# Kernel optimization log

Hardware: AMD Instinct MI355X
Metric: run time of the kernel (lower is better)

Reference implementation:

```python
import jax, jax.numpy as jnp
import numpy as np

B, C, H, W = 8, 256, 32, 32
N = H * W  # 1024; conv1 maps C -> N channels so all bmms are [B,N,N]


def setup_inputs() -> dict:
    key = jax.random.key(0)
    ks = jax.random.split(key, 11)
    s = 0.02  # weight scale to keep softmax logits in a sane range
    return {
        "x":     jax.random.normal(ks[0], (B, C, H, W), jnp.float32),
        "w1":    jax.random.normal(ks[1], (N, C), jnp.float32) * s,
        "b1":    jax.random.normal(ks[2], (N,), jnp.float32) * s,
        "wq":    jax.random.normal(ks[3], (N, N), jnp.float32) * s,
        "bq":    jax.random.normal(ks[4], (N,), jnp.float32) * s,
        "wv":    jax.random.normal(ks[5], (N, N), jnp.float32) * s,
        "bv":    jax.random.normal(ks[6], (N,), jnp.float32) * s,
        "w2":    jax.random.normal(ks[7], (C, N), jnp.float32) * s,
        "b2":    jax.random.normal(ks[8], (C,), jnp.float32) * s,
        "alpha": jax.random.normal(ks[9], (1,), jnp.float32),
        "beta":  jax.random.normal(ks[10], (1,), jnp.float32),
    }


def reference(x, w1, b1, wq, bq, wv, bv, w2, b2, alpha, beta):
    b, c, h, w = x.shape
    n = h * w
    # 1x1 convs as channel matmuls
    x1 = jnp.einsum('bchw,nc->bnhw', x, w1) + b1[None, :, None, None]  # [B,N,H,W]
    g = (jnp.einsum('bnhw,mn->bmhw', x1, wq) + bq[None, :, None, None]).reshape(b, n, n)
    r = (jnp.einsum('bnhw,mn->bmhw', x1, wv) + bv[None, :, None, None]).reshape(b, n, n)
    xf = x1.reshape(b, n, n)          # m^T in the torch code: [B, N_chan, HW]
    m = xf.transpose(0, 2, 1)         # m: [B, HW, N_chan]
    # spatial attention: z_s = softmax(m^T @ g)
    z_s = jax.nn.softmax(jnp.matmul(xf, g), axis=-1)            # [B,N,N]
    # channel attention: z_c = softmax(g^T @ m)
    z_c = jax.nn.softmax(jnp.matmul(g.transpose(0, 2, 1), m), axis=-1)  # [B,N,N]
    p_s = jnp.matmul(z_s, r)                                    # [B,N,HW]
    p_c = jnp.matmul(z_c, m).transpose(0, 2, 1)                 # [B,N,HW]
    p = (alpha[0] * p_s + beta[0] * p_c).reshape(b, n, h, w)
    out = jnp.einsum('bnhw,cn->bchw', p, w2) + b2[None, :, None, None]
    return out
```

## Files before the change

### kernel.cpp

```cpp
#include <hip/hip_runtime.h>
#include <hip/hip_bf16.h>


typedef __attribute__((ext_vector_type(4))) float f4;
typedef __attribute__((ext_vector_type(8))) short s8;
typedef __attribute__((ext_vector_type(4))) unsigned short us4;
typedef __attribute__((ext_vector_type(8))) unsigned short us8;

__device__ __forceinline__ unsigned short f2bf(float f) {
    __hip_bfloat16 h = __float2bfloat16(f);
    return __builtin_bit_cast(unsigned short, h);
}
__device__ __forceinline__ float bf2f(unsigned short u) {
    unsigned int x = ((unsigned int)u) << 16;
    return __builtin_bit_cast(float, x);
}

#define GAS(p) ((const __attribute__((address_space(1))) unsigned int*)(p))
#define LAS(p) ((__attribute__((address_space(3))) unsigned int*)(p))

__global__ __launch_bounds__(256) void prep(
    const float* __restrict__ w1, const float* __restrict__ wq,
    const float* __restrict__ wv, const float* __restrict__ w2,
    unsigned short* __restrict__ w1b, unsigned short* __restrict__ wqb,
    unsigned short* __restrict__ wvb, unsigned short* __restrict__ w2b,
    const float* __restrict__ bq, const float* __restrict__ bv,
    float* __restrict__ biasqv,
    const float* __restrict__ x, unsigned short* __restrict__ xT)
{
    __shared__ float tl[32][33];
    if (blockIdx.x < 2562) {
        long i = (long)blockIdx.x * 256 + threadIdx.x;
        if (i >= 655360) {
            long j = i - 655360;
            if (j < 512) {
                f4 v = (j < 256) ? ((const f4*)bq)[j] : ((const f4*)bv)[j - 256];
                ((f4*)biasqv)[j] = v;
            }
            return;
        }
        const float* src; unsigned short* dst; long base;
        if (i < 65536)               { src = w1; dst = w1b; base = 0; }
        else if (i < 65536+262144)   { src = wq; dst = wqb; base = 65536; }
        else if (i < 65536+524288)   { src = wv; dst = wvb; base = 65536+262144; }
        else                         { src = w2; dst = w2b; base = 65536+524288; }
        long j = i - base;
        f4 v = ((const f4*)src)[j];
        us4 o;
        #pragma unroll
        for (int k = 0; k < 4; ++k) o[k] = f2bf(v[k]);
        ((us4*)dst)[j] = o;
    } else {
        const int idx = blockIdx.x - 2562;
        const int q0 = (idx & 31) * 32;
        const int c0 = ((idx >> 5) & 7) * 32;
        const int b  = idx >> 8;
        const int tx = threadIdx.x & 31, ty = threadIdx.x >> 5;
        #pragma unroll
        for (int j = 0; j < 4; ++j)
            tl[ty + j*8][tx] = x[((long)(b*256 + c0 + ty + j*8))*1024 + q0 + tx];
        __syncthreads();
        #pragma unroll
        for (int j = 0; j < 4; ++j)
            xT[((long)(b*1024 + q0 + ty + j*8))*256 + c0 + tx] = f2bf(tl[tx][ty + j*8]);
    }
}

template<int BIAS, int SPLIT>
__global__ __launch_bounds__(512, 2) void gemm8p(
    const unsigned short* __restrict__ A0, const unsigned short* __restrict__ Bt0,
    int lda, int ldb,
    void* __restrict__ Cv0, void* __restrict__ Cv1, int ldc,
    const float* __restrict__ bias)
{
    constexpr int NT = 16;
    __shared__ __align__(16) unsigned short As[2][2][8192];
    __shared__ __align__(16) unsigned short Bs[2][2][8192];

    const int gx = gridDim.x, gy = gridDim.y;
    const int nwg = gx * gy;
    int d = blockIdx.x + gx * blockIdx.y;
    int swz = (d & 7) * (nwg >> 3) + (d >> 3);
    const int bx = swz % gx;
    const int by = swz / gx;

    const int m0 = by * 256;
    const int n0 = bx * 256;
    const int t  = threadIdx.x;
    const int w  = t >> 6, l = t & 63;
    const int wr = w >> 2, wc = w & 3;
    const int lr = l & 15, lg = l >> 4;

    const unsigned short* Asrc = A0  + (long)m0 * lda;
    const unsigned short* Bsrc = Bt0 + (long)n0 * ldb;

    const int rl4 = l >> 2;
    const int gsw = ((l & 3) ^ ((l >> 3) & 3)) * 8;
    const int rsw = (lr >> 1) & 3;

    auto stage = [&](const unsigned short* src, int ld_, unsigned short* slot,
                     int sp, int kh) {
        #pragma unroll
        for (int i = 0; i < 2; ++i) {
            const int rb = i*128 + w*16;
            __builtin_amdgcn_global_load_lds(
                GAS(src + (long)(rb + rl4)*ld_ + sp*64 + kh*32 + gsw),
                LAS(slot + rb*32), 16, 0, 0);
        }
    };

    f4 acc[8][4];
    #pragma unroll
    for (int i = 0; i < 8; ++i)
        #pragma unroll
        for (int j = 0; j < 4; ++j) acc[i][j] = (f4){0.f, 0.f, 0.f, 0.f};

    s8 aF[4], bF[4];
    auto rdA = [&](int db, int kh, int mh) {
        #pragma unroll
        for (int m = 0; m < 4; ++m) {
            const int R = wr*128 + mh*64 + m*16 + lr;
            aF[m] = *(const s8*)&As[db][kh][R*32 + ((lg ^ rsw) * 8)];
        }
    };
    auto rdB = [&](int db, int kh) {
        #pragma unroll
        for (int n = 0; n < 4; ++n) {
            const int R = wc*64 + n*16 + lr;
            bF[n] = *(const s8*)&Bs[db][kh][R*32 + ((lg ^ rsw) * 8)];
        }
    };

#define MM8(MH)                                                                  \
    __builtin_amdgcn_s_setprio(1);                                               \
    _Pragma("unroll")                                                            \
    for (int m_ = 0; m_ < 4; ++m_)                                               \
        _Pragma("unroll")                                                        \
        for (int n_ = 0; n_ < 4; ++n_)                                           \
            acc[(MH)*4 + m_][n_] = __builtin_amdgcn_mfma_f32_16x16x32_bf16(      \
                aF[m_], bF[n_], acc[(MH)*4 + m_][n_], 0, 0, 0);                  \
    __builtin_amdgcn_s_setprio(0);

#define PH8(DB, KH, MH, RB, STG, VM)                                             \
    rdA(DB, KH, MH);                                                             \
    if (RB) rdB(DB, KH);                                                         \
    STG;                                                                         \
    __builtin_amdgcn_sched_barrier(0);                                           \
    __builtin_amdgcn_s_barrier();                                                \
    asm volatile("s_waitcnt lgkmcnt(0)" ::: "memory");                           \
    __builtin_amdgcn_sched_barrier(0);                                           \
    MM8(MH);                                                                     \
    VM;                                                                          \
    __builtin_amdgcn_s_barrier();

    stage(Asrc, lda, &As[0][0][0], 0, 0);
    stage(Bsrc, ldb, &Bs[0][0][0], 0, 0);
    stage(Asrc, lda, &As[0][1][0], 0, 1);
    stage(Bsrc, ldb, &Bs[0][1][0], 0, 1);
    stage(Asrc, lda, &As[1][0][0], 1, 0);
    stage(Bsrc, ldb, &Bs[1][0][0], 1, 0);
    asm volatile("s_waitcnt vmcnt(4)" ::: "memory");
    __builtin_amdgcn_sched_barrier(0);
    __builtin_amdgcn_s_barrier();

    for (int j = 0; j < NT/2; ++j) {
        const int tb = 2*j + 1;
        const int t2 = (2*j + 2) & (NT - 1);
        const int t3 = (2*j + 3) & (NT - 1);
        PH8(0,0,0, 1, stage(Asrc, lda, &As[1][1][0], tb, 1), (void)0)
        PH8(0,0,1, 0, stage(Bsrc, ldb, &Bs[1][1][0], tb, 1), (void)0)
        PH8(0,1,0, 1, stage(Asrc, lda, &As[0][0][0], t2, 0), (void)0)
        PH8(0,1,1, 0, stage(Bsrc, ldb, &Bs[0][0][0], t2, 0),
            asm volatile("s_waitcnt vmcnt(4)" ::: "memory"))
        PH8(1,0,0, 1, stage(Asrc, lda, &As[0][1][0], t2, 1), (void)0)
        PH8(1,0,1, 0, stage(Bsrc, ldb, &Bs[0][1][0], t2, 1), (void)0)
        PH8(1,1,0, 1, stage(Asrc, lda, &As[1][0][0], t3, 0), (void)0)
        PH8(1,1,1, 0, stage(Bsrc, ldb, &Bs[1][0][0], t3, 0),
            asm volatile("s_waitcnt vmcnt(4)" ::: "memory"))
    }
#undef PH8
#undef MM8

    void* Cd = Cv0; int nbase = n0;
    if (SPLIT && n0 >= 1024) { Cd = Cv1; nbase = n0 - 1024; }

    const int rbase = lg * 4;
    #pragma unroll
    for (int mi = 0; mi < 8; ++mi) {
        #pragma unroll
        for (int n = 0; n < 4; ++n) {
            const int row  = m0 + wr*128 + mi*16 + rbase;
            const int col  = nbase + wc*64 + n*16 + lr;
            const int bcol = n0    + wc*64 + n*16 + lr;
            #pragma unroll
            for (int j = 0; j < 4; ++j) {
                float v = acc[mi][n][j];
                if (BIAS == 2) v += bias[bcol];
                ((unsigned short*)Cd)[(long)(row + j)*ldc + col] = f2bf(v);
            }
        }
    }
}

template<int BIAS, int OUTF32, int STATS>
__global__ __launch_bounds__(512, 2) void gemm256(
    const unsigned short* __restrict__ A0, const unsigned short* __restrict__ Bt0,
    long sA, long sB, int lda, int ldb,
    void* __restrict__ Cv0, long sC, int ldc,
    const float* __restrict__ bias, int nt1,
    float* __restrict__ csp, float* __restrict__ rsp,
    unsigned short* __restrict__ Et)
{
    __shared__ __align__(16) unsigned short As[3][16384];
    __shared__ __align__(16) unsigned short Bs[3][8192];

    const int gx = gridDim.x, gy = gridDim.y;
    const int nwg = gx * gy * gridDim.z;
    int d = blockIdx.x + gx * (blockIdx.y + gy * blockIdx.z);
    int swz = (d & 7) * (nwg >> 3) + (d >> 3);
    const int bx = swz % gx; int tq = swz / gx;
    const int by = tq % gy;  const int bz = tq / gy;

    const int b  = bz;
    const int m0 = by * 256;
    const int n0 = bx * 128;
    const int t  = threadIdx.x;
    const int w  = t >> 6, l = t & 63;
    const int wr = w >> 1, wc = w & 1;
    const int lr = l & 15, lg = l >> 4;

    const unsigned short* A0b = A0  + (long)b * sA;
    const unsigned short* B0b = Bt0 + (long)b * sB;

    const int rl  = l >> 3;
    const int gsw = ((l & 7) ^ (rl & 7)) * 8;

    const int NT = nt1;

    auto stageA = [&](int sp, int bf) {
        const int kt = sp * 64;
        #pragma unroll
        for (int i = 0; i < 4; ++i) {
            const int rb = w*32 + i*8;
            __builtin_amdgcn_global_load_lds(GAS(A0b + (long)(m0 + rb + rl)*lda + kt + gsw),
                                             LAS(&As[bf][rb*64]), 16, 0, 0);
        }
    };
    auto stageB = [&](int sp, int bf) {
        const int kt = sp * 64;
        #pragma unroll
        for (int i = 0; i < 2; ++i) {
            const int rb = w*16 + i*8;
            __builtin_amdgcn_global_load_lds(GAS(B0b + (long)(n0 + rb + rl)*ldb + kt + gsw),
                                             LAS(&Bs[bf][rb*64]), 16, 0, 0);
        }
    };

    f4 acc[4][4];
    #pragma unroll
    for (int i = 0; i < 4; ++i)
        #pragma unroll
        for (int j = 0; j < 4; ++j) acc[i][j] = (f4){0.f, 0.f, 0.f, 0.f};

    stageA(0, 0); stageB(0, 0);
    stageA(1, 1); stageB(1, 1);
    asm volatile("s_waitcnt vmcnt(6)" ::: "memory");
    __builtin_amdgcn_sched_barrier(0);
    __builtin_amdgcn_s_barrier();

    s8 a0[4], b0[4], a1f[4], b1f[4];

    #pragma unroll
    for (int m = 0; m < 4; ++m) {
        const int R = wr*64 + m*16 + lr;
        a0[m] = *(const s8*)&As[0][R*64 + ((lg ^ (R & 7)) * 8)];
    }
    #pragma unroll
    for (int n = 0; n < 4; ++n) {
        const int R = wc*64 + n*16 + lr;
        b0[n] = *(const s8*)&Bs[0][R*64 + ((lg ^ (R & 7)) * 8)];
    }
    asm volatile("s_waitcnt lgkmcnt(0)" ::: "memory");
    __builtin_amdgcn_sched_barrier(0);

    int buf = 0;
    for (int s = 0; s < NT; ++s) {
        int bn = buf + 2; if (bn >= 3) bn -= 3;
        int bx1 = buf + 1; if (bx1 >= 3) bx1 -= 3;

        #pragma unroll
        for (int m = 0; m < 4; ++m) {
            const int R = wr*64 + m*16 + lr;
            a1f[m] = *(const s8*)&As[buf][R*64 + (((4 + lg) ^ (R & 7)) * 8)];
        }
        #pragma unroll
        for (int n = 0; n < 4; ++n) {
            const int R = wc*64 + n*16 + lr;
            b1f[n] = *(const s8*)&Bs[buf][R*64 + (((4 + lg) ^ (R & 7)) * 8)];
        }
        if (s + 2 < NT) stageA(s + 2, bn);
        __builtin_amdgcn_s_setprio(1);
        #pragma unroll
        for (int m = 0; m < 4; ++m)
            #pragma unroll
            for (int n = 0; n < 4; ++n)
                acc[m][n] = __builtin_amdgcn_mfma_f32_16x16x32_bf16(a0[m], b0[n], acc[m][n], 0, 0, 0);
        __builtin_amdgcn_s_setprio(0);
        asm volatile("s_waitcnt lgkmcnt(0)" ::: "memory");
        __builtin_amdgcn_sched_barrier(0);

        if (s + 1 < NT) {
            if (s + 2 < NT) asm volatile("s_waitcnt vmcnt(4)" ::: "memory");
            else            asm volatile("s_waitcnt vmcnt(0)" ::: "memory");
            __builtin_amdgcn_sched_barrier(0);
            __builtin_amdgcn_s_barrier();
            #pragma unroll
            for (int m = 0; m < 4; ++m) {
                const int R = wr*64 + m*16 + lr;
                a0[m] = *(const s8*)&As[bx1][R*64 + ((lg ^ (R & 7)) * 8)];
            }
            #pragma unroll
            for (int n = 0; n < 4; ++n) {
                const int R = wc*64 + n*16 + lr;
                b0[n] = *(const s8*)&Bs[bx1][R*64 + ((lg ^ (R & 7)) * 8)];
            }
            if (s + 2 < NT) stageB(s + 2, bn);
            __builtin_amdgcn_s_setprio(1);
            #pragma unroll
            for (int m = 0; m < 4; ++m)
                #pragma unroll
                for (int n = 0; n < 4; ++n)
                    acc[m][n] = __builtin_amdgcn_mfma_f32_16x16x32_bf16(a1f[m], b1f[n], acc[m][n], 0, 0, 0);
            __builtin_amdgcn_s_setprio(0);
            asm volatile("s_waitcnt lgkmcnt(0)" ::: "memory");
            __builtin_amdgcn_sched_barrier(0);
        } else {
            __builtin_amdgcn_s_setprio(1);
            #pragma unroll
            for (int m = 0; m < 4; ++m)
                #pragma unroll
                for (int n = 0; n < 4; ++n)
                    acc[m][n] = __builtin_amdgcn_mfma_f32_16x16x32_bf16(a1f[m], b1f[n], acc[m][n], 0, 0, 0);
            __builtin_amdgcn_s_setprio(0);
        }

        buf = bx1;
    }

    const int rbase = lg * 4;

    if (STATS) {
        float csum[4] = {0.f, 0.f, 0.f, 0.f};
        float rsum[16];
        #pragma unroll
        for (int i = 0; i < 16; ++i) rsum[i] = 0.f;

        #pragma unroll
        for (int m = 0; m < 4; ++m) {
            #pragma unroll
            for (int n = 0; n < 4; ++n) {
                const int row = m0 + wr*64 + m*16 + rbase;
                const int col = n0 + wc*64 + n*16 + lr;
                us4 eo;
                #pragma unroll
                for (int j = 0; j < 4; ++j) {
                    float ev = __expf(acc[m][n][j]);
                    unsigned short bv = f2bf(ev);
                    ((unsigned short*)Cv0)[(long)b*sC + (long)(row + j)*ldc + col] = bv;
                    eo[j] = bv;
                    float evr = bf2f(bv);
                    csum[n] += evr;
                    rsum[m*4 + j] += evr;
                }
                *(us4*)&Et[(long)b*1048576 + (long)col*1024 + row] = eo;
            }
        }

        const int p = by*16 + wr*4 + lg;
        #pragma unroll
        for (int n = 0; n < 4; ++n) {
            const int col = n0 + wc*64 + n*16 + lr;
            csp[(long)p*8192 + b*1024 + col] = csum[n];
        }
        #pragma unroll
        for (int i = 0; i < 16; ++i) {
            #pragma unroll
            for (int off = 1; off < 16; off <<= 1)
                rsum[i] += __shfl_xor(rsum[i], off);
        }
        if (lr == 0) {
            const int p2 = bx*2 + wc;
            #pragma unroll
            for (int m = 0; m < 4; ++m)
                #pragma unroll
                for (int j = 0; j < 4; ++j) {
                    const int row = m0 + wr*64 + m*16 + rbase + j;
                    rsp[(long)(b*1024 + row)*16 + p2] = rsum[m*4 + j];
                }
        }
    } else {
        #pragma unroll
        for (int m = 0; m < 4; ++m) {
            #pragma unroll
            for (int n = 0; n < 4; ++n) {
                const int row = m0 + wr*64 + m*16 + rbase;
                const int col = n0 + wc*64 + n*16 + lr;
                #pragma unroll
                for (int j = 0; j < 4; ++j) {
                    float v = acc[m][n][j];
                    if (BIAS == 1) v += bias[row + j];
                    else if (BIAS == 2) v += bias[col];
                    const long idx = (long)b*sC + (long)(row + j)*ldc + col;
                    if (OUTF32) ((float*)Cv0)[idx] = v;
                    else ((unsigned short*)Cv0)[idx] = f2bf(v);
                }
            }
        }
    }
}

__global__ __launch_bounds__(512, 2) void gemm_x1(
    const unsigned short* __restrict__ w1b, const unsigned short* __restrict__ xTb,
    unsigned short* __restrict__ x1, unsigned short* __restrict__ x1T,
    const float* __restrict__ b1)
{
    constexpr int NT = 4;
    __shared__ __align__(16) unsigned short As[3][16384];
    __shared__ __align__(16) unsigned short Bs[3][8192];

    const int gx = gridDim.x, gy = gridDim.y;
    const int nwg = gx * gy * gridDim.z;
    int d = blockIdx.x + gx * (blockIdx.y + gy * blockIdx.z);
    int swz = (d & 7) * (nwg >> 3) + (d >> 3);
    const int bx = swz % gx; int tq = swz / gx;
    const int by = tq % gy;  const int bz = tq / gy;

    const bool roleA = (by < 4);
    const unsigned short* Ap;
    const unsigned short* Bp;
    unsigned short* Cp;
    int m0;
    if (roleA) {
        Ap = w1b;
        Bp = xTb + (long)bz * 262144;
        Cp = x1  + (long)bz * 1048576;
        m0 = by * 256;
    } else {
        Ap = xTb;
        Bp = w1b;
        Cp = x1T;
        m0 = (bz * 4 + (by - 4)) * 256;
    }
    const int n0 = bx * 128;
    const int t  = threadIdx.x;
    const int w  = t >> 6, l = t & 63;
    const int wr = w >> 1, wc = w & 1;
    const int lr = l & 15, lg = l >> 4;

    const int rl  = l >> 3;
    const int gsw = ((l & 7) ^ (rl & 7)) * 8;

    auto stageA = [&](int sp, int bf) {
        const int kt = sp * 64;
        #pragma unroll
        for (int i = 0; i < 4; ++i) {
            const int rb = w*32 + i*8;
            __builtin_amdgcn_global_load_lds(GAS(Ap + (long)(m0 + rb + rl)*256 + kt + gsw),
                                             LAS(&As[bf][rb*64]), 16, 0, 0);
        }
    };
    auto stageB = [&](int sp, int bf) {
        const int kt = sp * 64;
        #pragma unroll
        for (int i = 0; i < 2; ++i) {
            const int rb = w*16 + i*8;
            __builtin_amdgcn_global_load_lds(GAS(Bp + (long)(n0 + rb + rl)*256 + kt + gsw),
                                             LAS(&Bs[bf][rb*64]), 16, 0, 0);
        }
    };

    f4 acc[4][4];
    #pragma unroll
    for (int i = 0; i < 4; ++i)
        #pragma unroll
        for (int j = 0; j < 4; ++j) acc[i][j] = (f4){0.f, 0.f, 0.f, 0.f};

    stageA(0, 0); stageB(0, 0);
    stageA(1, 1); stageB(1, 1);
    asm volatile("s_waitcnt vmcnt(6)" ::: "memory");
    __builtin_amdgcn_sched_barrier(0);
    __builtin_amdgcn_s_barrier();

    s8 a0[4], b0[4], a1f[4], b1f[4];

    #pragma unroll
    for (int m = 0; m < 4; ++m) {
        const int R = wr*64 + m*16 + lr;
        a0[m] = *(const s8*)&As[0][R*64 + ((lg ^ (R & 7)) * 8)];
    }
    #pragma unroll
    for (int n = 0; n < 4; ++n) {
        const int R = wc*64 + n*16 + lr;
        b0[n] = *(const s8*)&Bs[0][R*64 + ((lg ^ (R & 7)) * 8)];
    }
    asm volatile("s_waitcnt lgkmcnt(0)" ::: "memory");
    __builtin_amdgcn_sched_barrier(0);

    int buf = 0;
    for (int s = 0; s < NT; ++s) {
        int bn = buf + 2; if (bn >= 3) bn -= 3;
        int bx1 = buf + 1; if (bx1 >= 3) bx1 -= 3;

        #pragma unroll
        for (int m = 0; m < 4; ++m) {
            const int R = wr*64 + m*16 + lr;
            a1f[m] = *(const s8*)&As[buf][R*64 + (((4 + lg) ^ (R & 7)) * 8)];
        }
        #pragma unroll
        for (int n = 0; n < 4; ++n) {
            const int R = wc*64 + n*16 + lr;
            b1f[n] = *(const s8*)&Bs[buf][R*64 + (((4 + lg) ^ (R & 7)) * 8)];
        }
        if (s + 2 < NT) stageA(s + 2, bn);
        __builtin_amdgcn_s_setprio(1);
        #pragma unroll
        for (int m = 0; m < 4; ++m)
            #pragma unroll
            for (int n = 0; n < 4; ++n)
                acc[m][n] = __builtin_amdgcn_mfma_f32_16x16x32_bf16(a0[m], b0[n], acc[m][n], 0, 0, 0);
        __builtin_amdgcn_s_setprio(0);
        asm volatile("s_waitcnt lgkmcnt(0)" ::: "memory");
        __builtin_amdgcn_sched_barrier(0);

        if (s + 1 < NT) {
            if (s + 2 < NT) asm volatile("s_waitcnt vmcnt(4)" ::: "memory");
            else            asm volatile("s_waitcnt vmcnt(0)" ::: "memory");
            __builtin_amdgcn_sched_barrier(0);
            __builtin_amdgcn_s_barrier();
            #pragma unroll
            for (int m = 0; m < 4; ++m) {
                const int R = wr*64 + m*16 + lr;
                a0[m] = *(const s8*)&As[bx1][R*64 + ((lg ^ (R & 7)) * 8)];
            }
            #pragma unroll
            for (int n = 0; n < 4; ++n) {
                const int R = wc*64 + n*16 + lr;
                b0[n] = *(const s8*)&Bs[bx1][R*64 + ((lg ^ (R & 7)) * 8)];
            }
            if (s + 2 < NT) stageB(s + 2, bn);
            __builtin_amdgcn_s_setprio(1);
            #pragma unroll
            for (int m = 0; m < 4; ++m)
                #pragma unroll
                for (int n = 0; n < 4; ++n)
                    acc[m][n] = __builtin_amdgcn_mfma_f32_16x16x32_bf16(a1f[m], b1f[n], acc[m][n], 0, 0, 0);
            __builtin_amdgcn_s_setprio(0);
            asm volatile("s_waitcnt lgkmcnt(0)" ::: "memory");
            __builtin_amdgcn_sched_barrier(0);
        } else {
            __builtin_amdgcn_s_setprio(1);
            #pragma unroll
            for (int m = 0; m < 4; ++m)
                #pragma unroll
                for (int n = 0; n < 4; ++n)
                    acc[m][n] = __builtin_amdgcn_mfma_f32_16x16x32_bf16(a1f[m], b1f[n], acc[m][n], 0, 0, 0);
            __builtin_amdgcn_s_setprio(0);
        }

        buf = bx1;
    }

    const int rbase = lg * 4;
    #pragma unroll
    for (int m = 0; m < 4; ++m) {
        #pragma unroll
        for (int n = 0; n < 4; ++n) {
            const int row = m0 + wr*64 + m*16 + rbase;
            const int col = n0 + wc*64 + n*16 + lr;
            const float cb = roleA ? 0.f : b1[col];
            #pragma unroll
            for (int j = 0; j < 4; ++j) {
                float v = acc[m][n][j] + (roleA ? b1[(row + j) & 1023] : cb);
                Cp[(long)(row + j)*1024 + col] = f2bf(v);
            }
        }
    }
}

__global__ __launch_bounds__(512, 2) void gemm_dual2(
    const unsigned short* __restrict__ A0, const unsigned short* __restrict__ Bt0,
    const unsigned short* __restrict__ A1, const unsigned short* __restrict__ Bt1,
    const float* __restrict__ rs, const float* __restrict__ cs,
    const float* __restrict__ alpha_p, const float* __restrict__ beta_p,
    unsigned short* __restrict__ C)
{
    constexpr int NT = 32;
    __shared__ __align__(16) unsigned short As[3][16384];
    __shared__ __align__(16) unsigned short Bs[3][8192];

    const int gx = gridDim.x, gy = gridDim.y;
    const int nwg = gx * gy * gridDim.z;
    int d = blockIdx.x + gx * (blockIdx.y + gy * blockIdx.z);
    int swz = (d & 7) * (nwg >> 3) + (d >> 3);
    const int bx = swz % gx; int tq = swz / gx;
    const int by = tq % gy;  const int bz = tq / gy;

    const int b  = bz;
    const int m0 = by * 256;
    const int n0 = bx * 128;
    const int t  = threadIdx.x;
    const int w  = t >> 6, l = t & 63;
    const int wr = w >> 1, wc = w & 1;
    const int lr = l & 15, lg = l >> 4;

    const unsigned short* A0b = A0  + (long)b * 1048576;
    const unsigned short* B0b = Bt0 + (long)b * 1048576;
    const unsigned short* A1b = A1  + (long)b * 1048576;
    const unsigned short* B1b = Bt1 + (long)b * 1048576;

    const int rl  = l >> 3;
    const int gsw = ((l & 7) ^ (rl & 7)) * 8;

    auto stageA = [&](int sp, int bf) {
        const unsigned short* Ap = (sp >= 16) ? A1b : A0b;
        const int kt = ((sp >= 16) ? sp - 16 : sp) * 64;
        #pragma unroll
        for (int i = 0; i < 4; ++i) {
            const int rb = w*32 + i*8;
            __builtin_amdgcn_global_load_lds(GAS(Ap + (long)(m0 + rb + rl)*1024 + kt + gsw),
                                             LAS(&As[bf][rb*64]), 16, 0, 0);
        }
    };
    auto stageB = [&](int sp, int bf) {
        const unsigned short* Bp = (sp >= 16) ? B1b : B0b;
        const int kt = ((sp >= 16) ? sp - 16 : sp) * 64;
        #pragma unroll
        for (int i = 0; i < 2; ++i) {
            const int rb = w*16 + i*8;
            __builtin_amdgcn_global_load_lds(GAS(Bp + (long)(n0 + rb + rl)*1024 + kt + gsw),
                                             LAS(&Bs[bf][rb*64]), 16, 0, 0);
        }
    };

    f4 acc1[4][4], acc2[4][4];
    #pragma unroll
    for (int i = 0; i < 4; ++i)
        #pragma unroll
        for (int j = 0; j < 4; ++j) {
            acc1[i][j] = (f4){0.f, 0.f, 0.f, 0.f};
            acc2[i][j] = (f4){0.f, 0.f, 0.f, 0.f};
        }

    stageA(0, 0); stageB(0, 0);
    stageA(1, 1); stageB(1, 1);
    asm volatile("s_waitcnt vmcnt(6)" ::: "memory");
    __builtin_amdgcn_sched_barrier(0);
    __builtin_amdgcn_s_barrier();

    s8 a0[4], b0[4], a1f[4], b1f[4];

    #pragma unroll
    for (int m = 0; m < 4; ++m) {
        const int R = wr*64 + m*16 + lr;
        a0[m] = *(const s8*)&As[0][R*64 + ((lg ^ (R & 7)) * 8)];
    }
    #pragma unroll
    for (int n = 0; n < 4; ++n) {
        const int R = wc*64 + n*16 + lr;
        b0[n] = *(const s8*)&Bs[0][R*64 + ((lg ^ (R & 7)) * 8)];
    }
    asm volatile("s_waitcnt lgkmcnt(0)" ::: "memory");
    __builtin_amdgcn_sched_barrier(0);

#define DUAL_BODY(ACC)                                                            \
    {                                                                             \
        int bn = buf + 2; if (bn >= 3) bn -= 3;                                   \
        int bx1 = buf + 1; if (bx1 >= 3) bx1 -= 3;                                \
        _Pragma("unroll")                                                         \
        for (int m = 0; m < 4; ++m) {                                             \
            const int R = wr*64 + m*16 + lr;                                      \
            a1f[m] = *(const s8*)&As[buf][R*64 + (((4 + lg) ^ (R & 7)) * 8)];     \
        }                                                                         \
        _Pragma("unroll")                                                         \
        for (int n = 0; n < 4; ++n) {                                             \
            const int R = wc*64 + n*16 + lr;                                      \
            b1f[n] = *(const s8*)&Bs[buf][R*64 + (((4 + lg) ^ (R & 7)) * 8)];     \
        }                                                                         \
        if (s + 2 < NT) stageA(s + 2, bn);                                        \
        __builtin_amdgcn_s_setprio(1);                                            \
        _Pragma("unroll")                                                         \
        for (int m = 0; m < 4; ++m)                                               \
            _Pragma("unroll")                                                     \
            for (int n = 0; n < 4; ++n)                                           \
                ACC[m][n] = __builtin_amdgcn_mfma_f32_16x16x32_bf16(a0[m], b0[n], ACC[m][n], 0, 0, 0); \
        __builtin_amdgcn_s_setprio(0);                                            \
        asm volatile("s_waitcnt lgkmcnt(0)" ::: "memory");                        \
        __builtin_amdgcn_sched_barrier(0);                                        \
        if (s + 1 < NT) {                                                         \
            if (s + 2 < NT) asm volatile("s_waitcnt vmcnt(4)" ::: "memory");      \
            else            asm volatile("s_waitcnt vmcnt(0)" ::: "memory");      \
            __builtin_amdgcn_sched_barrier(0);                                    \
            __builtin_amdgcn_s_barrier();                                         \
            _Pragma("unroll")                                                     \
            for (int m = 0; m < 4; ++m) {                                         \
                const int R = wr*64 + m*16 + lr;                                  \
                a0[m] = *(const s8*)&As[bx1][R*64 + ((lg ^ (R & 7)) * 8)];        \
            }                                                                     \
            _Pragma("unroll")                                                     \
            for (int n = 0; n < 4; ++n) {                                         \
                const int R = wc*64 + n*16 + lr;                                  \
                b0[n] = *(const s8*)&Bs[bx1][R*64 + ((lg ^ (R & 7)) * 8)];        \
            }                                                                     \
            if (s + 2 < NT) stageB(s + 2, bn);                                    \
            __builtin_amdgcn_s_setprio(1);                                        \
            _Pragma("unroll")                                                     \
            for (int m = 0; m < 4; ++m)                                           \
                _Pragma("unroll")                                                 \
                for (int n = 0; n < 4; ++n)                                       \
                    ACC[m][n] = __builtin_amdgcn_mfma_f32_16x16x32_bf16(a1f[m], b1f[n], ACC[m][n], 0, 0, 0); \
            __builtin_amdgcn_s_setprio(0);                                        \
            asm volatile("s_waitcnt lgkmcnt(0)" ::: "memory");                    \
            __builtin_amdgcn_sched_barrier(0);                                    \
        } else {                                                                  \
            __builtin_amdgcn_s_setprio(1);                                        \
            _Pragma("unroll")                                                     \
            for (int m = 0; m < 4; ++m)                                           \
                _Pragma("unroll")                                                 \
                for (int n = 0; n < 4; ++n)                                       \
                    ACC[m][n] = __builtin_amdgcn_mfma_f32_16x16x32_bf16(a1f[m], b1f[n], ACC[m][n], 0, 0, 0); \
            __builtin_amdgcn_s_setprio(0);                                        \
        }                                                                         \
        buf = bx1;                                                                \
    }

    int buf = 0;
    for (int s = 0; s < 16; ++s) DUAL_BODY(acc1)
    for (int s = 16; s < NT; ++s) DUAL_BODY(acc2)
#undef DUAL_BODY

    const float al = alpha_p[0], be = beta_p[0];
    const int rbase = lg * 4;
    float rscv[4];
    #pragma unroll
    for (int n = 0; n < 4; ++n)
        rscv[n] = al / rs[b*1024 + n0 + wc*64 + n*16 + lr];

    #pragma unroll
    for (int m = 0; m < 4; ++m) {
        #pragma unroll
        for (int j = 0; j < 4; ++j) {
            const int row = m0 + wr*64 + m*16 + rbase + j;
            const float csc = be / cs[b*1024 + row];
            #pragma unroll
            for (int n = 0; n < 4; ++n) {
                const int col = n0 + wc*64 + n*16 + lr;
                float v = acc1[m][n][j]*rscv[n] + acc2[m][n][j]*csc;
                C[(long)b*1048576 + (long)row*1024 + col] = f2bf(v);
            }
        }
    }
}

template<int BIAS, int OUTF32, int NT1, int NBUF>
__global__ __launch_bounds__(256) void gemm_pipe(
    const unsigned short* __restrict__ A0, const unsigned short* __restrict__ Bt0,
    long sA, long sB, int lda, int ldb,
    void* __restrict__ Cv0, long sC, int ldc,
    const float* __restrict__ bias)
{
    constexpr int NT = NT1;
    __shared__ __align__(16) unsigned short As[NBUF][4096];
    __shared__ __align__(16) unsigned short Bs[NBUF][4096];

    const int gx = gridDim.x, gy = gridDim.y;
    const int nwg = gx * gy * gridDim.z;
    int d = blockIdx.x + gx * (blockIdx.y + gy * blockIdx.z);
    int swz = (d & 7) * (nwg >> 3) + (d >> 3);
    const int bx = swz % gx; int tq = swz / gx;
    const int by = tq % gy;  const int bz = tq / gy;

    const int b  = bz;
    const int m0 = by * 128;
    const int n0 = bx * 128;
    const int t  = threadIdx.x;
    const int w  = t >> 6, l = t & 63;
    const int wr = w >> 1, wc = w & 1;
    const int lr = l & 15;

    const unsigned short* A0b = A0  + (long)b * sA;
    const unsigned short* B0b = Bt0 + (long)b * sB;

    const int rA   = w*32 + (l >> 2);
    const int cswz = ((l & 3) ^ ((l >> 3) & 3)) * 8;
    const int swzr = (((l >> 4) ^ ((lr >> 1) & 3)) * 8);

    f4 acc[4][4];
    #pragma unroll
    for (int i = 0; i < 4; ++i)
        #pragma unroll
        for (int j = 0; j < 4; ++j) acc[i][j] = (f4){0.f, 0.f, 0.f, 0.f};

    auto stage = [&](int sp, int bf) {
        const int kt = sp * 32;
        __builtin_amdgcn_global_load_lds(GAS(A0b + (long)(m0 + rA     )*lda + kt + cswz), LAS(&As[bf][w*1024      ]), 16, 0, 0);
        __builtin_amdgcn_global_load_lds(GAS(A0b + (long)(m0 + rA + 16)*lda + kt + cswz), LAS(&As[bf][w*1024 + 512]), 16, 0, 0);
        __builtin_amdgcn_global_load_lds(GAS(B0b + (long)(n0 + rA     )*ldb + kt + cswz), LAS(&Bs[bf][w*1024      ]), 16, 0, 0);
        __builtin_amdgcn_global_load_lds(GAS(B0b + (long)(n0 + rA + 16)*ldb + kt + cswz), LAS(&Bs[bf][w*1024 + 512]), 16, 0, 0);
    };

    #pragma unroll
    for (int dpl = 0; dpl < NBUF - 1; ++dpl) stage(dpl, dpl);

    int buf = 0;
    for (int s = 0; s < NT; ++s) {
        if (NBUF >= 4 && s + 2 < NT) asm volatile("s_waitcnt vmcnt(8)" ::: "memory");
        else if (s + 1 < NT)         asm volatile("s_waitcnt vmcnt(4)" ::: "memory");
        else                         asm volatile("s_waitcnt vmcnt(0)" ::: "memory");
        __builtin_amdgcn_s_barrier();
        __builtin_amdgcn_sched_barrier(0);

        s8 aF[4], bF[4];
        #pragma unroll
        for (int m = 0; m < 4; ++m) aF[m] = *(const s8*)&As[buf][(wr*64 + m*16 + lr)*32 + swzr];
        #pragma unroll
        for (int n = 0; n < 4; ++n) bF[n] = *(const s8*)&Bs[buf][(wc*64 + n*16 + lr)*32 + swzr];

        if (s + NBUF - 1 < NT) {
            int bn = buf + NBUF - 1; if (bn >= NBUF) bn -= NBUF;
            stage(s + NBUF - 1, bn);
        }

        __builtin_amdgcn_s_setprio(1);
        #pragma unroll
        for (int m = 0; m < 4; ++m)
            #pragma unroll
            for (int n = 0; n < 4; ++n)
                acc[m][n] = __builtin_amdgcn_mfma_f32_16x16x32_bf16(aF[m], bF[n], acc[m][n], 0, 0, 0);
        __builtin_amdgcn_s_setprio(0);

        if (++buf == NBUF) buf = 0;
    }

    const int rbase = (l >> 4) * 4;
    #pragma unroll
    for (int m = 0; m < 4; ++m) {
        #pragma unroll
        for (int n = 0; n < 4; ++n) {
            const int row = m0 + wr*64 + m*16 + rbase;
            const int col = n0 + wc*64 + n*16 + lr;
            #pragma unroll
            for (int j = 0; j < 4; ++j) {
                float v = acc[m][n][j];
                if (BIAS == 1) v += bias[row + j];
                else if (BIAS == 2) v += bias[col];
                const long idx = (long)b*sC + (long)(row + j)*ldc + col;
                if (OUTF32) ((float*)Cv0)[idx] = v;
                else ((unsigned short*)Cv0)[idx] = f2bf(v);
            }
        }
    }
}

__global__ __launch_bounds__(256) void stats_reduce(
    const float* __restrict__ csp, const float* __restrict__ rsp,
    float* __restrict__ cs, float* __restrict__ rs)
{
    if (blockIdx.x < 32) {
        const int q = blockIdx.x * 256 + threadIdx.x;
        float s = 0.f;
        #pragma unroll
        for (int p = 0; p < 64; ++p) s += csp[(long)p*8192 + q];
        cs[q] = s;
    } else {
        const int row = (blockIdx.x - 32) * 256 + threadIdx.x;
        float s = 0.f;
        #pragma unroll
        for (int i = 0; i < 4; ++i) {
            f4 v = *(const f4*)&rsp[(long)row*16 + i*4];
            s += v[0] + v[1] + v[2] + v[3];
        }
        rs[row] = s;
    }
}

extern "C" void kernel_launch(void* const* d_in, const int* in_sizes, int n_in,
                              void* d_out, int out_size, void* d_ws, size_t ws_size,
                              hipStream_t stream)
{
    const float* x     = (const float*)d_in[0];
    const float* w1    = (const float*)d_in[1];
    const float* b1    = (const float*)d_in[2];
    const float* wq    = (const float*)d_in[3];
    const float* bq    = (const float*)d_in[4];
    const float* wv    = (const float*)d_in[5];
    const float* bv    = (const float*)d_in[6];
    const float* w2    = (const float*)d_in[7];
    const float* b2    = (const float*)d_in[8];
    const float* alpha = (const float*)d_in[9];
    const float* beta  = (const float*)d_in[10];
    float* out = (float*)d_out;

    char* ws = (char*)d_ws;
    size_t off = 0;
    auto alloc = [&](size_t bytes) -> void* {
        void* p = ws + off; off += (bytes + 255) & ~(size_t)255; return p;
    };
    unsigned short* w1b   = (unsigned short*)alloc(1024L*256*2);
    unsigned short* wqvb  = (unsigned short*)alloc(2048L*1024*2);
    unsigned short* w2b   = (unsigned short*)alloc(256L*1024*2);
    float*          biasqv= (float*)alloc(2048L*4);
    float*          cspv  = (float*)alloc(64L*8192*4);
    float*          rspv  = (float*)alloc(8192L*16*4);
    float*          csv   = (float*)alloc(8L*1024*4);
    float*          rsv   = (float*)alloc(8L*1024*4);
    unsigned short* xTb   = (unsigned short*)alloc(8L*1024*256*2);
    unsigned short* x1b   = (unsigned short*)alloc(8L*1024*1024*2);
    unsigned short* x1tb  = (unsigned short*)alloc(8L*1024*1024*2);
    unsigned short* gtb   = (unsigned short*)alloc(8L*1024*1024*2);
    unsigned short* rtb   = (unsigned short*)alloc(8L*1024*1024*2);
    unsigned short* Etb   = (unsigned short*)alloc(8L*1024*1024*2);
    unsigned short* Ptb   = (unsigned short*)alloc(8L*1024*1024*2);
    unsigned short* Eb  = x1tb;

    const long S1M = 1048576;

    prep<<<4610, 256, 0, stream>>>(w1, wq, wv, w2, w1b, wqvb, wqvb + S1M, w2b,
                                   bq, bv, biasqv, x, xTb);

    gemm_x1<<<dim3(8, 8, 8), 512, 0, stream>>>(w1b, xTb, x1b, x1tb, b1);
    gemm8p<2,1><<<dim3(8, 32), 512, 0, stream>>>(
        x1tb, wqvb, 1024, 1024, gtb, rtb, 1024, biasqv);
    gemm256<0,0,1><<<dim3(8, 4, 8), 512, 0, stream>>>(
        x1b, gtb, S1M, S1M, 1024, 1024, Eb, S1M, 1024, nullptr, 16, cspv, rspv, Etb);
    stats_reduce<<<64, 256, 0, stream>>>(cspv, rspv, csv, rsv);
    gemm_dual2<<<dim3(8, 4, 8), 512, 0, stream>>>(
        rtb, Eb, Etb, x1b, rsv, csv, alpha, beta, Ptb);
    gemm_pipe<1,1,32,4><<<dim3(8, 2, 8), 256, 0, stream>>>(
        w2b, Ptb, 0, S1M, 1024, 1024, out, 262144, 1024, b2);
}
```

Before: 165.9 us.

## Move E transpose out of GEMM epilogue into separate tiled transpose kernel

The stats GEMM no longer writes the transposed exp matrix with strided 8-byte stores, and it no longer does the intra-wave shuffle reduction of row sums. Partial row sums are now written per lane into a wider buffer and reduced in stats_reduce with wave shuffles. A new LDS-tiled transpose kernel builds Et from E and writes it into the gt buffer, which is dead at that point. The aim is to cut uncoalesced scattered stores and epilogue register pressure, at the cost of an extra kernel launch and an extra full read and write of E.

```diff
diff --git a/kernel.cpp b/kernel.cpp
--- a/kernel.cpp
+++ b/kernel.cpp
@@ -208,8 +208,7 @@
     long sA, long sB, int lda, int ldb,
     void* __restrict__ Cv0, long sC, int ldc,
     const float* __restrict__ bias, int nt1,
-    float* __restrict__ csp, float* __restrict__ rsp,
-    unsigned short* __restrict__ Et)
+    float* __restrict__ csp, float* __restrict__ rsp)
 {
     __shared__ __align__(16) unsigned short As[3][16384];
     __shared__ __align__(16) unsigned short Bs[3][8192];
@@ -348,74 +347,54 @@
     }
 
     const int rbase = lg * 4;
-
-    if (STATS) {
-        float csum[4] = {0.f, 0.f, 0.f, 0.f};
-        float rsum[16];
-        #pragma unroll
-        for (int i = 0; i < 16; ++i) rsum[i] = 0.f;
-
-        #pragma unroll
-        for (int m = 0; m < 4; ++m) {
-            #pragma unroll
-            for (int n = 0; n < 4; ++n) {
-                const int row = m0 + wr*64 + m*16 + rbase;
-                const int col = n0 + wc*64 + n*16 + lr;
-                us4 eo;
-                #pragma unroll
-                for (int j = 0; j < 4; ++j) {
-                    float ev = __expf(acc[m][n][j]);
+    float csum[4] = {0.f, 0.f, 0.f, 0.f};
+    float rsum[16];
+    #pragma unroll
+    for (int i = 0; i < 16; ++i) rsum[i] = 0.f;
+
+    #pragma unroll
+    for (int m = 0; m < 4; ++m) {
+        #pragma unroll
+        for (int n = 0; n < 4; ++n) {
+            const int row  = m0 + wr*64 + m*16 + rbase;
+            const int col  = n0 + wc*64 + n*16 + lr;
+            #pragma unroll
+            for (int j = 0; j < 4; ++j) {
+                float v = acc[m][n][j];
+                if (BIAS == 1) v += bias[row + j];
+                else if (BIAS == 2) v += bias[col];
+                const long idx = (long)b*sC + (long)(row + j)*ldc + col;
+                if (STATS) {
+                    float ev = __expf(v);
                     unsigned short bv = f2bf(ev);
-                    ((unsigned short*)Cv0)[(long)b*sC + (long)(row + j)*ldc + col] = bv;
-                    eo[j] = bv;
+                    ((unsigned short*)Cv0)[idx] = bv;
                     float evr = bf2f(bv);
                     csum[n] += evr;
                     rsum[m*4 + j] += evr;
+                } else if (OUTF32) {
+                    ((float*)Cv0)[idx] = v;
+                } else {
+                    ((unsigned short*)Cv0)[idx] = f2bf(v);
                 }
-                *(us4*)&Et[(long)b*1048576 + (long)col*1024 + row] = eo;
-            }
-        }
-
+            }
+        }
+    }
+
+    if (STATS) {
         const int p = by*16 + wr*4 + lg;
         #pragma unroll
         for (int n = 0; n < 4; ++n) {
             const int col = n0 + wc*64 + n*16 + lr;
             csp[(long)p*8192 + b*1024 + col] = csum[n];
         }
-        #pragma unroll
-        for (int i = 0; i < 16; ++i) {
-            #pragma unroll
-            for (int off = 1; off < 16; off <<= 1)
-                rsum[i] += __shfl_xor(rsum[i], off);
-        }
-        if (lr == 0) {
-            const int p2 = bx*2 + wc;
-            #pragma unroll
-            for (int m = 0; m < 4; ++m)
-                #pragma unroll
-                for (int j = 0; j < 4; ++j) {
-                    const int row = m0 + wr*64 + m*16 + rbase + j;
-                    rsp[(long)(b*1024 + row)*16 + p2] = rsum[m*4 + j];
-                }
-        }
-    } else {
-        #pragma unroll
-        for (int m = 0; m < 4; ++m) {
-            #pragma unroll
-            for (int n = 0; n < 4; ++n) {
-                const int row = m0 + wr*64 + m*16 + rbase;
-                const int col = n0 + wc*64 + n*16 + lr;
-                #pragma unroll
-                for (int j = 0; j < 4; ++j) {
-                    float v = acc[m][n][j];
-                    if (BIAS == 1) v += bias[row + j];
-                    else if (BIAS == 2) v += bias[col];
-                    const long idx = (long)b*sC + (long)(row + j)*ldc + col;
-                    if (OUTF32) ((float*)Cv0)[idx] = v;
-                    else ((unsigned short*)Cv0)[idx] = f2bf(v);
-                }
-            }
-        }
+        const int p2 = bx*32 + wc*16 + lr;
+        #pragma unroll
+        for (int m = 0; m < 4; ++m)
+            #pragma unroll
+            for (int j = 0; j < 4; ++j) {
+                const int row = m0 + wr*64 + m*16 + rbase + j;
+                rsp[(long)(b*1024 + row)*256 + p2] = rsum[m*4 + j];
+            }
     }
 }
 
@@ -872,14 +851,46 @@
         for (int p = 0; p < 64; ++p) s += csp[(long)p*8192 + q];
         cs[q] = s;
     } else {
-        const int row = (blockIdx.x - 32) * 256 + threadIdx.x;
-        float s = 0.f;
+        const int blk = blockIdx.x - 32;
+        const int w = threadIdx.x >> 6, l = threadIdx.x & 63;
         #pragma unroll
         for (int i = 0; i < 4; ++i) {
-            f4 v = *(const f4*)&rsp[(long)row*16 + i*4];
-            s += v[0] + v[1] + v[2] + v[3];
-        }
-        rs[row] = s;
+            const int row = blk*16 + w*4 + i;
+            f4 v = *(const f4*)&rsp[(long)row*256 + l*4];
+            float s = v[0] + v[1] + v[2] + v[3];
+            #pragma unroll
+            for (int off = 32; off; off >>= 1) s += __shfl_xor(s, off);
+            if (l == 0) rs[row] = s;
+        }
+    }
+}
+
+__global__ __launch_bounds__(256) void et_trans(
+    const unsigned short* __restrict__ E, unsigned short* __restrict__ Et)
+{
+    __shared__ unsigned short tile[64][65];
+    const int b  = blockIdx.z;
+    const int i0 = blockIdx.x * 64;
+    const int q0 = blockIdx.y * 64;
+    const int t  = threadIdx.x;
+    const int ch = t & 7, r = t >> 3;
+    const unsigned short* Eb = E + (long)b * 1048576;
+    #pragma unroll
+    for (int pp = 0; pp < 2; ++pp) {
+        const int rr = r + pp*32;
+        us8 v = *(const us8*)&Eb[(long)(i0 + rr)*1024 + q0 + ch*8];
+        #pragma unroll
+        for (int e = 0; e < 8; ++e) tile[rr][ch*8 + e] = v[e];
+    }
+    __syncthreads();
+    unsigned short* Etb = Et + (long)b * 1048576;
+    #pragma unroll
+    for (int pp = 0; pp < 2; ++pp) {
+        const int qr = r + pp*32;
+        us8 o;
+        #pragma unroll
+        for (int e = 0; e < 8; ++e) o[e] = tile[ch*8 + e][qr];
+        *(us8*)&Etb[(long)(q0 + qr)*1024 + i0 + ch*8] = o;
     }
 }
 
@@ -910,7 +921,7 @@
     unsigned short* w2b   = (unsigned short*)alloc(256L*1024*2);
     float*          biasqv= (float*)alloc(2048L*4);
     float*          cspv  = (float*)alloc(64L*8192*4);
-    float*          rspv  = (float*)alloc(8192L*16*4);
+    float*          rspv  = (float*)alloc(8192L*256*4);
     float*          csv   = (float*)alloc(8L*1024*4);
     float*          rsv   = (float*)alloc(8L*1024*4);
     unsigned short* xTb   = (unsigned short*)alloc(8L*1024*256*2);
@@ -918,9 +929,9 @@
     unsigned short* x1tb  = (unsigned short*)alloc(8L*1024*1024*2);
     unsigned short* gtb   = (unsigned short*)alloc(8L*1024*1024*2);
     unsigned short* rtb   = (unsigned short*)alloc(8L*1024*1024*2);
-    unsigned short* Etb   = (unsigned short*)alloc(8L*1024*1024*2);
     unsigned short* Ptb   = (unsigned short*)alloc(8L*1024*1024*2);
     unsigned short* Eb  = x1tb;
+    unsigned short* Etb = gtb;
 
     const long S1M = 1048576;
 
@@ -931,8 +942,9 @@
     gemm8p<2,1><<<dim3(8, 32), 512, 0, stream>>>(
         x1tb, wqvb, 1024, 1024, gtb, rtb, 1024, biasqv);
     gemm256<0,0,1><<<dim3(8, 4, 8), 512, 0, stream>>>(
-        x1b, gtb, S1M, S1M, 1024, 1024, Eb, S1M, 1024, nullptr, 16, cspv, rspv, Etb);
-    stats_reduce<<<64, 256, 0, stream>>>(cspv, rspv, csv, rsv);
+        x1b, gtb, S1M, S1M, 1024, 1024, Eb, S1M, 1024, nullptr, 16, cspv, rspv);
+    stats_reduce<<<544, 256, 0, stream>>>(cspv, rspv, csv, rsv);
+    et_trans<<<dim3(16, 16, 8), 256, 0, stream>>>(Eb, Etb);
     gemm_dual2<<<dim3(8, 4, 8), 512, 0, stream>>>(
         rtb, Eb, Etb, x1b, rsv, csv, alpha, beta, Ptb);
     gemm_pipe<1,1,32,4><<<dim3(8, 2, 8), 256, 0, stream>>>(
```

Result: slower. 171.0 us (+3.1%).
